# Performance work log

Measured on AMD Instinct MI355X. Metric: run time of the kernel, lower is better.

The kernel has to match this reference:

```python
import jax, jax.numpy as jnp
import numpy as np

N = 100000
E = 1600000
IN_C, HID_C, OUT_C = 128, 128, 64


def setup_inputs() -> dict:
    key = jax.random.key(0)
    ks = jax.random.split(key, 8)
    x = jax.random.normal(ks[0], (N, IN_C), dtype=jnp.float32)
    edge_index = jax.random.randint(ks[1], (2, E), 0, N, dtype=jnp.int64)

    def glorot(k, fan_in, fan_out):
        s = jnp.sqrt(6.0 / (fan_in + fan_out))
        return jax.random.uniform(k, (fan_in, fan_out), jnp.float32, -s, s)

    W1 = glorot(ks[2], IN_C, HID_C)
    b1 = jnp.zeros((HID_C,), jnp.float32)
    W2 = glorot(ks[3], HID_C, HID_C)
    b2 = jnp.zeros((HID_C,), jnp.float32)
    W3 = glorot(ks[4], HID_C, OUT_C)
    b3 = jnp.zeros((OUT_C,), jnp.float32)
    return {"x": x, "edge_index": edge_index,
            "W1": W1, "b1": b1, "W2": W2, "b2": b2, "W3": W3, "b3": b3}


def _gcn_norm(row, col, n_nodes):
    # symmetric normalization, add_self_loops=False (PyG gcn_norm)
    deg = jax.ops.segment_sum(jnp.ones(row.shape[0], jnp.float32), col, num_segments=n_nodes)
    dinv = jnp.where(deg > 0, jax.lax.rsqrt(jnp.maximum(deg, 1.0)), 0.0)
    dinv = jnp.where(deg > 0, deg ** -0.5, 0.0)
    return dinv[row] * dinv[col]  # [E]


def _gcn_conv(x, row, col, norm, W, b):
    h = x @ W                                # [N, F_out] dense GEMM first (PyG order)
    msg = h[row] * norm[:, None]             # gather + scale, [E, F_out]
    out = jax.ops.segment_sum(msg, col, num_segments=x.shape[0])  # scatter-add
    return out + b


def reference(x, edge_index, W1, b1, W2, b2, W3, b3):
    row, col = edge_index[0], edge_index[1]
    norm = _gcn_norm(row, col, x.shape[0])
    h = jax.nn.relu(_gcn_conv(x, row, col, norm, W1, b1))   # dropout is identity in eval
    h = jax.nn.relu(_gcn_conv(h, row, col, norm, W2, b2))
    out = _gcn_conv(h, row, col, norm, W3, b3)
    return out
```

## Files before the change

### kernel.cpp

```cpp
#include <hip/hip_runtime.h>
#include <hip/hip_bf16.h>
#include <hip/hip_fp16.h>


#define K_DIM 128
#define SCAN_CHUNK 1024

typedef _Float16 f16x8 __attribute__((ext_vector_type(8)));
typedef float f32x4 __attribute__((ext_vector_type(4)));
struct h2s { _Float16 x, y; };

static inline long long cdiv_ll(long long a, long long b) { return (a + b - 1) / b; }

__global__ __launch_bounds__(256) void count_kernel(const int* __restrict__ col, int* __restrict__ cnt, int E) {
    int e = blockIdx.x * 256 + threadIdx.x;
    if (e < E) atomicAdd(&cnt[col[e]], 1);
}

__global__ __launch_bounds__(256) void dinv_kernel(const int* __restrict__ cnt, float* __restrict__ dinv, int N) {
    int n = blockIdx.x * 256 + threadIdx.x;
    if (n < N) {
        int d = cnt[n];
        dinv[n] = (d > 0) ? (1.0f / sqrtf((float)d)) : 0.0f;
    }
}

__global__ __launch_bounds__(256) void scan1_kernel(const int* __restrict__ cnt, int* __restrict__ off,
                                                    int* __restrict__ bsum, int N) {
    __shared__ int lds[256];
    const int t = threadIdx.x;
    const int base = blockIdx.x * SCAN_CHUNK;
    int v[4], s = 0;
#pragma unroll
    for (int j = 0; j < 4; ++j) {
        int i = base + t * 4 + j;
        v[j] = (i < N) ? cnt[i] : 0;
        s += v[j];
    }
    lds[t] = s;
    __syncthreads();
    for (int d = 1; d < 256; d <<= 1) {
        int x = (t >= d) ? lds[t - d] : 0;
        __syncthreads();
        lds[t] += x;
        __syncthreads();
    }
    int excl = lds[t] - s;
    if (t == 255) bsum[blockIdx.x] = lds[255];
    int run = excl;
#pragma unroll
    for (int j = 0; j < 4; ++j) {
        int i = base + t * 4 + j;
        if (i < N) off[i] = run;
        run += v[j];
    }
}

__global__ __launch_bounds__(256) void scan2_kernel(int* __restrict__ bsum, int G, int* __restrict__ off,
                                                    int N, int E) {
    __shared__ int lds[256];
    const int t = threadIdx.x;
    int s = (t < G) ? bsum[t] : 0;
    lds[t] = s;
    __syncthreads();
    for (int d = 1; d < 256; d <<= 1) {
        int x = (t >= d) ? lds[t - d] : 0;
        __syncthreads();
        lds[t] += x;
        __syncthreads();
    }
    if (t < G) bsum[t] = lds[t] - s;
    if (t == 0) off[N] = E;
}

__global__ __launch_bounds__(256) void scan3_kernel(int* __restrict__ off, const int* __restrict__ bsum, int N) {
    int add = bsum[blockIdx.x];
    const int base = blockIdx.x * SCAN_CHUNK;
#pragma unroll
    for (int j = 0; j < 4; ++j) {
        int i = base + threadIdx.x * 4 + j;
        if (i < N) off[i] += add;
    }
}

__global__ __launch_bounds__(256) void fill_kernel(const int* __restrict__ row, const int* __restrict__ col,
                                                   const int* __restrict__ off, int* __restrict__ cur,
                                                   int* __restrict__ csr_row, int E) {
    int e = blockIdx.x * 256 + threadIdx.x;
    if (e < E) {
        int c = col[e];
        int p = atomicAdd(&cur[c], 1);
        csr_row[off[c] + p] = row[e];
    }
}

template <int COUT>
__global__ __launch_bounds__(256) void pack_w_kernel(const float* __restrict__ W, _Float16* __restrict__ Wp) {
    constexpr int NT = COUT / 16;
    int t = blockIdx.x * 256 + threadIdx.x;
    if (t >= 4 * NT * 64) return;
    int lane = t & 63;
    int nt = (t >> 6) % NT;
    int kt = t / (64 * NT);
    int c = lane & 15, q = lane >> 4;
    f16x8 v;
#pragma unroll
    for (int j = 0; j < 8; ++j) {
        int k = kt * 32 + q * 8 + j;
        v[j] = (_Float16)W[k * COUT + nt * 16 + c];
    }
    *(f16x8*)&Wp[(size_t)t * 8] = v;
}

template <int COUT, bool AF16>
__global__ __launch_bounds__(256) void gemm_mfma(const void* __restrict__ Av, const _Float16* __restrict__ Wp,
                                                 const float* __restrict__ dinv, _Float16* __restrict__ Cmat, int M) {
    constexpr int NT = COUT / 16;
    constexpr int NFRAG = 4 * NT * 64;
    __shared__ _Float16 Wlds[NFRAG * 8];

    const int t = threadIdx.x;
    for (int i = t; i < NFRAG; i += 256)
        *(f16x8*)&Wlds[(size_t)i * 8] = *(const f16x8*)&Wp[(size_t)i * 8];
    __syncthreads();

    const int lane = t & 63;
    const int wave = t >> 6;
    const int c = lane & 15;
    const int q = lane >> 4;
    const int row_base = blockIdx.x * 128 + wave * 32;

    f32x4 acc[2][NT];
#pragma unroll
    for (int rt = 0; rt < 2; ++rt)
#pragma unroll
        for (int nt = 0; nt < NT; ++nt) {
            acc[rt][nt][0] = 0.f; acc[rt][nt][1] = 0.f;
            acc[rt][nt][2] = 0.f; acc[rt][nt][3] = 0.f;
        }

#pragma unroll
    for (int kt = 0; kt < 4; ++kt) {
        f16x8 a[2];
#pragma unroll
        for (int rt = 0; rt < 2; ++rt) {
            int r = row_base + rt * 16 + c;
            r = (r < M) ? r : (M - 1);
            if (AF16) {
                a[rt] = *(const f16x8*)((const _Float16*)Av + (size_t)r * K_DIM + kt * 32 + q * 8);
            } else {
                const float* ap = (const float*)Av + (size_t)r * K_DIM + kt * 32 + q * 8;
                float4 v0 = *(const float4*)ap;
                float4 v1 = *(const float4*)(ap + 4);
                f16x8 av;
                av[0] = (_Float16)v0.x; av[1] = (_Float16)v0.y;
                av[2] = (_Float16)v0.z; av[3] = (_Float16)v0.w;
                av[4] = (_Float16)v1.x; av[5] = (_Float16)v1.y;
                av[6] = (_Float16)v1.z; av[7] = (_Float16)v1.w;
                a[rt] = av;
            }
        }
#pragma unroll
        for (int nt = 0; nt < NT; ++nt) {
            f16x8 b = *(const f16x8*)&Wlds[(size_t)((kt * NT + nt) * 64 + lane) * 8];
            acc[0][nt] = __builtin_amdgcn_mfma_f32_16x16x32_f16(a[0], b, acc[0][nt], 0, 0, 0);
            acc[1][nt] = __builtin_amdgcn_mfma_f32_16x16x32_f16(a[1], b, acc[1][nt], 0, 0, 0);
        }
    }

#pragma unroll
    for (int rt = 0; rt < 2; ++rt)
#pragma unroll
        for (int reg = 0; reg < 4; ++reg) {
            int row = row_base + rt * 16 + q * 4 + reg;
            if (row < M) {
                float dv = dinv[row];
#pragma unroll
                for (int nt = 0; nt < NT; ++nt)
                    Cmat[(size_t)row * COUT + nt * 16 + c] = (_Float16)(acc[rt][nt][reg] * dv);
            }
        }
}

template <int C, bool RELU, typename OutT>
__global__ __launch_bounds__(256) void gather_kernel(const _Float16* __restrict__ g, const int* __restrict__ off,
                                                     const int* __restrict__ csr_row, const float* __restrict__ dinv,
                                                     const float* __restrict__ bias, OutT* __restrict__ out, int N) {
    const int wave = (blockIdx.x * 256 + threadIdx.x) >> 6;
    const int lane = threadIdx.x & 63;
    if (wave >= N) return;
    const int s0 = off[wave];
    const int s1 = off[wave + 1];
    const float dv = dinv[wave];

    if (C == 128) {
        float ax = 0.f, ay = 0.f;
        int s = s0;
        for (; s + 4 <= s1; s += 4) {
            int r0 = csr_row[s], r1 = csr_row[s + 1], r2 = csr_row[s + 2], r3 = csr_row[s + 3];
            h2s v0 = *(const h2s*)&g[(size_t)r0 * 128 + lane * 2];
            h2s v1 = *(const h2s*)&g[(size_t)r1 * 128 + lane * 2];
            h2s v2 = *(const h2s*)&g[(size_t)r2 * 128 + lane * 2];
            h2s v3 = *(const h2s*)&g[(size_t)r3 * 128 + lane * 2];
            ax += (float)v0.x + (float)v1.x + (float)v2.x + (float)v3.x;
            ay += (float)v0.y + (float)v1.y + (float)v2.y + (float)v3.y;
        }
        for (; s < s1; ++s) {
            h2s v = *(const h2s*)&g[(size_t)csr_row[s] * 128 + lane * 2];
            ax += (float)v.x;
            ay += (float)v.y;
        }
        float ox = ax * dv + bias[lane * 2 + 0];
        float oy = ay * dv + bias[lane * 2 + 1];
        if (RELU) { ox = fmaxf(ox, 0.f); oy = fmaxf(oy, 0.f); }
        if constexpr (sizeof(OutT) == 2) {
            h2s o; o.x = (_Float16)ox; o.y = (_Float16)oy;
            *(h2s*)((_Float16*)out + (size_t)wave * 128 + lane * 2) = o;
        } else {
            float2 o = make_float2(ox, oy);
            *(float2*)((float*)out + (size_t)wave * 128 + lane * 2) = o;
        }
    } else {
        float a0 = 0.f;
        int s = s0;
        for (; s + 4 <= s1; s += 4) {
            int r0 = csr_row[s], r1 = csr_row[s + 1], r2 = csr_row[s + 2], r3 = csr_row[s + 3];
            a0 += (float)g[(size_t)r0 * 64 + lane] + (float)g[(size_t)r1 * 64 + lane] +
                  (float)g[(size_t)r2 * 64 + lane] + (float)g[(size_t)r3 * 64 + lane];
        }
        for (; s < s1; ++s) a0 += (float)g[(size_t)csr_row[s] * 64 + lane];
        float o = a0 * dv + bias[lane];
        if (RELU) o = fmaxf(o, 0.f);
        ((OutT*)out)[(size_t)wave * 64 + lane] = (OutT)o;
    }
}

extern "C" void kernel_launch(void* const* d_in, const int* in_sizes, int n_in,
                              void* d_out, int out_size, void* d_ws, size_t ws_size,
                              hipStream_t stream) {
    const float* x  = (const float*)d_in[0];
    const int*   ei = (const int*)d_in[1];
    const float* W1 = (const float*)d_in[2];
    const float* b1 = (const float*)d_in[3];
    const float* W2 = (const float*)d_in[4];
    const float* b2 = (const float*)d_in[5];
    const float* W3 = (const float*)d_in[6];
    const float* b3 = (const float*)d_in[7];

    const int N = in_sizes[0] / 128;
    const int E = in_sizes[1] / 2;
    const int* row = ei;
    const int* col = ei + E;
    const int G = (int)cdiv_ll(N, SCAN_CHUNK);

    char* wsb = (char*)d_ws;
    int*      cnt     = (int*)wsb;      wsb += (size_t)N * 4;
    float*    dinv    = (float*)wsb;    wsb += (size_t)N * 4;
    int*      off     = (int*)wsb;      wsb += (size_t)(N + 1) * 4;
    int*      bsum    = (int*)wsb;      wsb += 256 * 4;
    int*      csr_row = (int*)wsb;      wsb += (size_t)E * 4;
    wsb = (char*)((((uintptr_t)wsb) + 15) & ~(uintptr_t)15);
    _Float16* Wp1     = (_Float16*)wsb; wsb += 16384 * 2;
    _Float16* Wp2     = (_Float16*)wsb; wsb += 16384 * 2;
    _Float16* Wp3     = (_Float16*)wsb; wsb += 8192 * 2;
    _Float16* bufA    = (_Float16*)wsb; wsb += (size_t)N * 128 * 2;
    _Float16* bufB    = (_Float16*)wsb;
    float*    out     = (float*)d_out;

    hipMemsetAsync(cnt, 0, (size_t)N * 4, stream);
    count_kernel<<<cdiv_ll(E, 256), 256, 0, stream>>>(col, cnt, E);
    dinv_kernel<<<cdiv_ll(N, 256), 256, 0, stream>>>(cnt, dinv, N);
    scan1_kernel<<<G, 256, 0, stream>>>(cnt, off, bsum, N);
    scan2_kernel<<<1, 256, 0, stream>>>(bsum, G, off, N, E);
    scan3_kernel<<<G, 256, 0, stream>>>(off, bsum, N);
    hipMemsetAsync(cnt, 0, (size_t)N * 4, stream);
    fill_kernel<<<cdiv_ll(E, 256), 256, 0, stream>>>(row, col, off, cnt, csr_row, E);
    pack_w_kernel<128><<<8, 256, 0, stream>>>(W1, Wp1);
    pack_w_kernel<128><<<8, 256, 0, stream>>>(W2, Wp2);
    pack_w_kernel<64><<<4, 256, 0, stream>>>(W3, Wp3);

    const long long gemmBlocks   = cdiv_ll(N, 128);
    const long long gatherBlocks = cdiv_ll(N, 4);

    gemm_mfma<128, false><<<gemmBlocks, 256, 0, stream>>>(x, Wp1, dinv, bufA, N);
    gather_kernel<128, true, _Float16><<<gatherBlocks, 256, 0, stream>>>(bufA, off, csr_row, dinv, b1, bufB, N);

    gemm_mfma<128, true><<<gemmBlocks, 256, 0, stream>>>(bufB, Wp2, dinv, bufA, N);
    gather_kernel<128, true, _Float16><<<gatherBlocks, 256, 0, stream>>>(bufA, off, csr_row, dinv, b2, bufB, N);

    gemm_mfma<64, true><<<gemmBlocks, 256, 0, stream>>>(bufB, Wp3, dinv, bufA, N);
    gather_kernel<64, false, float><<<gatherBlocks, 256, 0, stream>>>(bufA, off, csr_row, dinv, b3, out, N);
}
```

Measured before the change: 561.9 us.

## Store features in 16-channel planes and gather per plane with edge-parallel lanes

Intermediate features move from row-major [N,128] to planar [C/16][N][16] fp16. The GEMM writes and reads this layout, and the gather kernels are split across 8 (or 4) feature planes, with 8 lanes per edge so each wave handles 8 edges at once, followed by a shuffle reduction. Each plane (about 3.2MB) is meant to fit in cache and raise the hit rate of the random gathers. In exchange, the csr_row indices are re-read once per plane. The CSR build also records each edge's atomic rank during counting, which removes the second memset and the atomics in the fill pass, at the cost of an extra E-sized workspace array.

```diff
diff --git a/kernel.cpp b/kernel.cpp
--- a/kernel.cpp
+++ b/kernel.cpp
@@ -12,9 +12,10 @@
 
 static inline long long cdiv_ll(long long a, long long b) { return (a + b - 1) / b; }
 
-__global__ __launch_bounds__(256) void count_kernel(const int* __restrict__ col, int* __restrict__ cnt, int E) {
+__global__ __launch_bounds__(256) void count_kernel(const int* __restrict__ col, int* __restrict__ cnt,
+                                                    int* __restrict__ rank, int E) {
     int e = blockIdx.x * 256 + threadIdx.x;
-    if (e < E) atomicAdd(&cnt[col[e]], 1);
+    if (e < E) rank[e] = atomicAdd(&cnt[col[e]], 1);
 }
 
 __global__ __launch_bounds__(256) void dinv_kernel(const int* __restrict__ cnt, float* __restrict__ dinv, int N) {
@@ -84,13 +85,12 @@
 }
 
 __global__ __launch_bounds__(256) void fill_kernel(const int* __restrict__ row, const int* __restrict__ col,
-                                                   const int* __restrict__ off, int* __restrict__ cur,
+                                                   const int* __restrict__ off, const int* __restrict__ rank,
                                                    int* __restrict__ csr_row, int E) {
     int e = blockIdx.x * 256 + threadIdx.x;
     if (e < E) {
-        int c = col[e];
-        int p = atomicAdd(&cur[c], 1);
-        csr_row[off[c] + p] = row[e];
+        int idx = off[col[e]] + rank[e];
+        __builtin_nontemporal_store(row[e], &csr_row[idx]);
     }
 }
 
@@ -147,7 +147,9 @@
             int r = row_base + rt * 16 + c;
             r = (r < M) ? r : (M - 1);
             if (AF16) {
-                a[rt] = *(const f16x8*)((const _Float16*)Av + (size_t)r * K_DIM + kt * 32 + q * 8);
+                const _Float16* Ap = (const _Float16*)Av;
+                int p = kt * 2 + (q >> 1);
+                a[rt] = *(const f16x8*)&Ap[((size_t)p * M + r) * 16 + (q & 1) * 8];
             } else {
                 const float* ap = (const float*)Av + (size_t)r * K_DIM + kt * 32 + q * 8;
                 float4 v0 = *(const float4*)ap;
@@ -177,61 +179,74 @@
                 float dv = dinv[row];
 #pragma unroll
                 for (int nt = 0; nt < NT; ++nt)
-                    Cmat[(size_t)row * COUT + nt * 16 + c] = (_Float16)(acc[rt][nt][reg] * dv);
+                    Cmat[((size_t)nt * M + row) * 16 + c] = (_Float16)(acc[rt][nt][reg] * dv);
             }
         }
 }
 
-template <int C, bool RELU, typename OutT>
-__global__ __launch_bounds__(256) void gather_kernel(const _Float16* __restrict__ g, const int* __restrict__ off,
-                                                     const int* __restrict__ csr_row, const float* __restrict__ dinv,
-                                                     const float* __restrict__ bias, OutT* __restrict__ out, int N) {
-    const int wave = (blockIdx.x * 256 + threadIdx.x) >> 6;
+__global__ __launch_bounds__(256) void gather_mid(const _Float16* __restrict__ g, const int* __restrict__ off,
+                                                  const int* __restrict__ csr_row, const float* __restrict__ dinv,
+                                                  const float* __restrict__ bias, _Float16* __restrict__ outp, int N) {
+    const int gp = blockIdx.x & 7;
+    const int node = (blockIdx.x >> 3) * 4 + (threadIdx.x >> 6);
+    if (node >= N) return;
     const int lane = threadIdx.x & 63;
-    if (wave >= N) return;
-    const int s0 = off[wave];
-    const int s1 = off[wave + 1];
-    const float dv = dinv[wave];
-
-    if (C == 128) {
-        float ax = 0.f, ay = 0.f;
-        int s = s0;
-        for (; s + 4 <= s1; s += 4) {
-            int r0 = csr_row[s], r1 = csr_row[s + 1], r2 = csr_row[s + 2], r3 = csr_row[s + 3];
-            h2s v0 = *(const h2s*)&g[(size_t)r0 * 128 + lane * 2];
-            h2s v1 = *(const h2s*)&g[(size_t)r1 * 128 + lane * 2];
-            h2s v2 = *(const h2s*)&g[(size_t)r2 * 128 + lane * 2];
-            h2s v3 = *(const h2s*)&g[(size_t)r3 * 128 + lane * 2];
-            ax += (float)v0.x + (float)v1.x + (float)v2.x + (float)v3.x;
-            ay += (float)v0.y + (float)v1.y + (float)v2.y + (float)v3.y;
-        }
-        for (; s < s1; ++s) {
-            h2s v = *(const h2s*)&g[(size_t)csr_row[s] * 128 + lane * 2];
-            ax += (float)v.x;
-            ay += (float)v.y;
-        }
-        float ox = ax * dv + bias[lane * 2 + 0];
-        float oy = ay * dv + bias[lane * 2 + 1];
-        if (RELU) { ox = fmaxf(ox, 0.f); oy = fmaxf(oy, 0.f); }
-        if constexpr (sizeof(OutT) == 2) {
-            h2s o; o.x = (_Float16)ox; o.y = (_Float16)oy;
-            *(h2s*)((_Float16*)out + (size_t)wave * 128 + lane * 2) = o;
-        } else {
-            float2 o = make_float2(ox, oy);
-            *(float2*)((float*)out + (size_t)wave * 128 + lane * 2) = o;
-        }
-    } else {
-        float a0 = 0.f;
-        int s = s0;
-        for (; s + 4 <= s1; s += 4) {
-            int r0 = csr_row[s], r1 = csr_row[s + 1], r2 = csr_row[s + 2], r3 = csr_row[s + 3];
-            a0 += (float)g[(size_t)r0 * 64 + lane] + (float)g[(size_t)r1 * 64 + lane] +
-                  (float)g[(size_t)r2 * 64 + lane] + (float)g[(size_t)r3 * 64 + lane];
-        }
-        for (; s < s1; ++s) a0 += (float)g[(size_t)csr_row[s] * 64 + lane];
-        float o = a0 * dv + bias[lane];
-        if (RELU) o = fmaxf(o, 0.f);
-        ((OutT*)out)[(size_t)wave * 64 + lane] = (OutT)o;
+    const int es = lane >> 3;
+    const int ch = lane & 7;
+    const int s1 = off[node + 1];
+    const _Float16* plane = g + (size_t)gp * N * 16;
+
+    float ax = 0.f, ay = 0.f;
+    for (int s = off[node] + es; s < s1; s += 8) {
+        int r = csr_row[s];
+        h2s v = *(const h2s*)&plane[(size_t)r * 16 + ch * 2];
+        ax += (float)v.x;
+        ay += (float)v.y;
+    }
+#pragma unroll
+    for (int d = 8; d < 64; d <<= 1) {
+        ax += __shfl_xor(ax, d, 64);
+        ay += __shfl_xor(ay, d, 64);
+    }
+    if (lane < 8) {
+        float dv = dinv[node];
+        float ox = fmaxf(ax * dv + bias[gp * 16 + ch * 2 + 0], 0.f);
+        float oy = fmaxf(ay * dv + bias[gp * 16 + ch * 2 + 1], 0.f);
+        h2s o; o.x = (_Float16)ox; o.y = (_Float16)oy;
+        *(h2s*)&outp[((size_t)gp * N + node) * 16 + ch * 2] = o;
+    }
+}
+
+__global__ __launch_bounds__(256) void gather_final(const _Float16* __restrict__ g, const int* __restrict__ off,
+                                                    const int* __restrict__ csr_row, const float* __restrict__ dinv,
+                                                    const float* __restrict__ bias, float* __restrict__ out, int N) {
+    const int gp = blockIdx.x & 3;
+    const int node = (blockIdx.x >> 2) * 4 + (threadIdx.x >> 6);
+    if (node >= N) return;
+    const int lane = threadIdx.x & 63;
+    const int es = lane >> 3;
+    const int ch = lane & 7;
+    const int s1 = off[node + 1];
+    const _Float16* plane = g + (size_t)gp * N * 16;
+
+    float ax = 0.f, ay = 0.f;
+    for (int s = off[node] + es; s < s1; s += 8) {
+        int r = csr_row[s];
+        h2s v = *(const h2s*)&plane[(size_t)r * 16 + ch * 2];
+        ax += (float)v.x;
+        ay += (float)v.y;
+    }
+#pragma unroll
+    for (int d = 8; d < 64; d <<= 1) {
+        ax += __shfl_xor(ax, d, 64);
+        ay += __shfl_xor(ay, d, 64);
+    }
+    if (lane < 8) {
+        float dv = dinv[node];
+        float2 o;
+        o.x = ax * dv + bias[gp * 16 + ch * 2 + 0];
+        o.y = ay * dv + bias[gp * 16 + ch * 2 + 1];
+        *(float2*)&out[(size_t)node * 64 + gp * 16 + ch * 2] = o;
     }
 }
 
@@ -258,6 +273,7 @@
     float*    dinv    = (float*)wsb;    wsb += (size_t)N * 4;
     int*      off     = (int*)wsb;      wsb += (size_t)(N + 1) * 4;
     int*      bsum    = (int*)wsb;      wsb += 256 * 4;
+    int*      rank    = (int*)wsb;      wsb += (size_t)E * 4;
     int*      csr_row = (int*)wsb;      wsb += (size_t)E * 4;
     wsb = (char*)((((uintptr_t)wsb) + 15) & ~(uintptr_t)15);
     _Float16* Wp1     = (_Float16*)wsb; wsb += 16384 * 2;
@@ -268,26 +284,26 @@
     float*    out     = (float*)d_out;
 
     hipMemsetAsync(cnt, 0, (size_t)N * 4, stream);
-    count_kernel<<<cdiv_ll(E, 256), 256, 0, stream>>>(col, cnt, E);
+    count_kernel<<<cdiv_ll(E, 256), 256, 0, stream>>>(col, cnt, rank, E);
     dinv_kernel<<<cdiv_ll(N, 256), 256, 0, stream>>>(cnt, dinv, N);
     scan1_kernel<<<G, 256, 0, stream>>>(cnt, off, bsum, N);
     scan2_kernel<<<1, 256, 0, stream>>>(bsum, G, off, N, E);
     scan3_kernel<<<G, 256, 0, stream>>>(off, bsum, N);
-    hipMemsetAsync(cnt, 0, (size_t)N * 4, stream);
-    fill_kernel<<<cdiv_ll(E, 256), 256, 0, stream>>>(row, col, off, cnt, csr_row, E);
+    fill_kernel<<<cdiv_ll(E, 256), 256, 0, stream>>>(row, col, off, rank, csr_row, E);
     pack_w_kernel<128><<<8, 256, 0, stream>>>(W1, Wp1);
     pack_w_kernel<128><<<8, 256, 0, stream>>>(W2, Wp2);
     pack_w_kernel<64><<<4, 256, 0, stream>>>(W3, Wp3);
 
-    const long long gemmBlocks   = cdiv_ll(N, 128);
-    const long long gatherBlocks = cdiv_ll(N, 4);
+    const long long gemmBlocks  = cdiv_ll(N, 128);
+    const long long gMidBlocks  = cdiv_ll(N, 4) * 8;
+    const long long gFinBlocks  = cdiv_ll(N, 4) * 4;
 
     gemm_mfma<128, false><<<gemmBlocks, 256, 0, stream>>>(x, Wp1, dinv, bufA, N);
-    gather_kernel<128, true, _Float16><<<gatherBlocks, 256, 0, stream>>>(bufA, off, csr_row, dinv, b1, bufB, N);
+    gather_mid<<<gMidBlocks, 256, 0, stream>>>(bufA, off, csr_row, dinv, b1, bufB, N);
 
     gemm_mfma<128, true><<<gemmBlocks, 256, 0, stream>>>(bufB, Wp2, dinv, bufA, N);
-    gather_kernel<128, true, _Float16><<<gatherBlocks, 256, 0, stream>>>(bufA, off, csr_row, dinv, b2, bufB, N);
+    gather_mid<<<gMidBlocks, 256, 0, stream>>>(bufA, off, csr_row, dinv, b2, bufB, N);
 
     gemm_mfma<64, true><<<gemmBlocks, 256, 0, stream>>>(bufB, Wp3, dinv, bufA, N);
-    gather_kernel<64, false, float><<<gatherBlocks, 256, 0, stream>>>(bufA, off, csr_row, dinv, b3, out, N);
-}
+    gather_final<<<gFinBlocks, 256, 0, stream>>>(bufA, off, csr_row, dinv, b3, out, N);
+}
```

After: 868.9 us. +54.7%, slower.
